# Performance work log

Hardware: AMD Instinct MI355X
Metric: run time of the kernel (lower is better)

Reference implementation:

```python
import jax, jax.numpy as jnp
import numpy as np

N, E, D_IN, D_HID, D_OUT = 50000, 600000, 128, 128, 64


def setup_inputs() -> dict:
    key = jax.random.key(0)
    ks = jax.random.split(key, 8)
    x = jax.random.normal(ks[0], (N, D_IN), dtype=jnp.float32)
    edge_index = jax.random.randint(ks[1], (2, E), 0, N, dtype=jnp.int64)
    def glorot(k, fan_in, fan_out):
        s = (6.0 / (fan_in + fan_out)) ** 0.5
        return jax.random.uniform(k, (fan_in, fan_out), jnp.float32, -s, s)
    return {
        "x": x,
        "W1": glorot(ks[2], D_IN, D_HID), "b1": jnp.zeros((D_HID,), jnp.float32),
        "W2": glorot(ks[3], D_HID, D_HID), "b2": jnp.zeros((D_HID,), jnp.float32),
        "W3": glorot(ks[4], D_HID, D_OUT), "b3": jnp.zeros((D_OUT,), jnp.float32),
        "edge_index": edge_index,
    }


def reference(x, W1, b1, W2, b2, W3, b3, edge_index):
    n = x.shape[0]
    # GCN with self-loops: A_hat = A + I, norm = D^-1/2 A_hat D^-1/2
    loops = jnp.arange(n, dtype=edge_index.dtype)
    row = jnp.concatenate([edge_index[0], loops])  # source nodes
    col = jnp.concatenate([edge_index[1], loops])  # target nodes
    deg = jax.ops.segment_sum(jnp.ones_like(col, dtype=x.dtype), col, num_segments=n)
    dinv = jnp.where(deg > 0, jax.lax.rsqrt(deg), 0.0)
    norm = dinv[row] * dinv[col]  # [E+N]

    def gcn_conv(h, W, b):
        hw = h @ W                                   # [N, out]
        msg = hw[row] * norm[:, None]                # [E+N, out] gather + scale
        return jax.ops.segment_sum(msg, col, num_segments=n) + b

    h = jax.nn.relu(gcn_conv(x, W1, b1))
    h = jax.nn.relu(gcn_conv(h, W2, b2))
    return gcn_conv(h, W3, b3)
```

## Files before the change

### kernel.cpp

```cpp
#include <hip/hip_runtime.h>
#include <hip/hip_bf16.h>
#include <hip/hip_fp16.h>


__device__ inline float4 h4_to_f4(float2 raw) {
    __half2 lo = *reinterpret_cast<__half2*>(&raw.x);
    __half2 hi = *reinterpret_cast<__half2*>(&raw.y);
    float2 a = __half22float2(lo);
    float2 b = __half22float2(hi);
    return make_float4(a.x, a.y, b.x, b.y);
}

__device__ inline float2 f4_to_h4(float4 v) {
    __half2 lo = __floats2half2_rn(v.x, v.y);
    __half2 hi = __floats2half2_rn(v.z, v.w);
    float2 r;
    r.x = *reinterpret_cast<float*>(&lo);
    r.y = *reinterpret_cast<float*>(&hi);
    return r;
}

__global__ __launch_bounds__(256) void zero_counts_kernel(int4* __restrict__ p, int n4) {
    int i = blockIdx.x * 256 + threadIdx.x;
    if (i < n4) p[i] = make_int4(0, 0, 0, 0);
}

__global__ void count_edges_kernel(const int* __restrict__ col, int* __restrict__ counts, int E) {
    int e = blockIdx.x * blockDim.x + threadIdx.x;
    if (e < E) atomicAdd(&counts[col[e]], 1);
}

__global__ __launch_bounds__(256) void block_sum_kernel(const int* __restrict__ counts,
                                                        int* __restrict__ blocksum, int n) {
    int i = blockIdx.x * 256 + threadIdx.x;
    int v = (i < n) ? counts[i] : 0;
    #pragma unroll
    for (int d = 1; d < 64; d <<= 1) v += __shfl_xor(v, d);
    __shared__ int ws[4];
    if ((threadIdx.x & 63) == 0) ws[threadIdx.x >> 6] = v;
    __syncthreads();
    if (threadIdx.x == 0) blocksum[blockIdx.x] = ws[0] + ws[1] + ws[2] + ws[3];
}

__global__ __launch_bounds__(256) void scan_sums_kernel(const int* __restrict__ blocksum,
                                                        int* __restrict__ blockoff,
                                                        int* __restrict__ offsets, int nb, int n) {
    int tid = threadIdx.x;
    int lane = tid & 63, wid = tid >> 6;
    int orig = (tid < nb) ? blocksum[tid] : 0;
    int v = orig;
    #pragma unroll
    for (int d = 1; d < 64; d <<= 1) {
        int u = __shfl_up(v, d);
        if (lane >= d) v += u;
    }
    __shared__ int ws[4];
    if (lane == 63) ws[wid] = v;
    __syncthreads();
    int add = 0;
    for (int w = 0; w < wid; ++w) add += ws[w];
    v += add;
    if (tid < nb) blockoff[tid] = v - orig;
    if (tid == 255) offsets[n] = v;
}

__global__ __launch_bounds__(256) void write_offsets_kernel(const int* __restrict__ counts,
                                                            const int* __restrict__ blockoff,
                                                            int* __restrict__ offsets,
                                                            int* __restrict__ cursor,
                                                            float* __restrict__ dinv, int n) {
    int tid = threadIdx.x;
    int i = blockIdx.x * 256 + tid;
    int lane = tid & 63, wid = tid >> 6;
    int c = (i < n) ? counts[i] : 0;
    int v = c;
    #pragma unroll
    for (int d = 1; d < 64; d <<= 1) {
        int u = __shfl_up(v, d);
        if (lane >= d) v += u;
    }
    __shared__ int ws[4];
    if (lane == 63) ws[wid] = v;
    __syncthreads();
    int add = 0;
    for (int w = 0; w < wid; ++w) add += ws[w];
    int incl = v + add;
    if (i < n) {
        offsets[i] = blockoff[blockIdx.x] + incl - c;
        cursor[i] = 0;
        dinv[i] = rsqrtf((float)(c + 1));
    }
}

__global__ void fill_csr_kernel(const int* __restrict__ row, const int* __restrict__ col,
                                const int* __restrict__ offsets, int* __restrict__ cursor,
                                const float* __restrict__ dinv,
                                int2* __restrict__ edges, int E) {
    int e = blockIdx.x * blockDim.x + threadIdx.x;
    if (e < E) {
        int c = col[e];
        int r = row[e];
        int pos = offsets[c] + atomicAdd(&cursor[c], 1);
        edges[pos] = make_int2(r, __float_as_int(dinv[r] * dinv[c]));
    }
}

template <int DO>
__global__ __launch_bounds__(256, 2) void gemm_kernel(const float* __restrict__ A,
                                                      const float* __restrict__ W,
                                                      __half* __restrict__ out, int n) {
    constexpr int K = 128;
    constexpr int COLTH = DO / 8;
    constexpr int ROWTH = 256 / COLTH;
    constexpr int R = 8;
    constexpr int BR = ROWTH * R;
    constexpr int HALF = DO / 2;

    __shared__ float Wl[K * DO];

    int tid = threadIdx.x;
    #pragma unroll
    for (int q = tid; q < K * DO / 4; q += 256) {
        ((float4*)Wl)[q] = ((const float4*)W)[q];
    }
    __syncthreads();

    int ct = tid % COLTH;
    int rt = tid / COLTH;
    int rb = blockIdx.x * BR + rt * R;

    const float4* A4 = (const float4*)A;

    int rowc[R];
    #pragma unroll
    for (int i = 0; i < R; ++i) {
        int row = rb + i;
        rowc[i] = (row < n) ? row : (n - 1);
    }

    float4 acc[R][2];
    #pragma unroll
    for (int i = 0; i < R; ++i) {
        acc[i][0].x = acc[i][0].y = acc[i][0].z = acc[i][0].w = 0.f;
        acc[i][1].x = acc[i][1].y = acc[i][1].z = acc[i][1].w = 0.f;
    }

    #pragma unroll 2
    for (int k4 = 0; k4 < K / 4; ++k4) {
        float4 areg[R];
        #pragma unroll
        for (int i = 0; i < R; ++i) {
            areg[i] = A4[(size_t)rowc[i] * (K / 4) + k4];
        }
        #pragma unroll
        for (int q = 0; q < 4; ++q) {
            int k = k4 * 4 + q;
            float4 w0 = *(const float4*)(Wl + k * DO + ct * 4);
            float4 w1 = *(const float4*)(Wl + k * DO + HALF + ct * 4);
            #pragma unroll
            for (int i = 0; i < R; ++i) {
                float a = (q == 0) ? areg[i].x : (q == 1) ? areg[i].y
                        : (q == 2) ? areg[i].z : areg[i].w;
                acc[i][0].x += a * w0.x; acc[i][0].y += a * w0.y;
                acc[i][0].z += a * w0.z; acc[i][0].w += a * w0.w;
                acc[i][1].x += a * w1.x; acc[i][1].y += a * w1.y;
                acc[i][1].z += a * w1.z; acc[i][1].w += a * w1.w;
            }
        }
    }

    #pragma unroll
    for (int i = 0; i < R; ++i) {
        int row = rb + i;
        if (row < n) {
            *(float2*)(out + (size_t)row * DO + ct * 4) = f4_to_h4(acc[i][0]);
            *(float2*)(out + (size_t)row * DO + HALF + ct * 4) = f4_to_h4(acc[i][1]);
        }
    }
}

template <int DO, bool RELU>
__global__ __launch_bounds__(256) void agg_kernel(const __half* __restrict__ hw,
                                                  const int* __restrict__ offsets,
                                                  const int2* __restrict__ edges,
                                                  const float* __restrict__ dinv,
                                                  const float* __restrict__ bias,
                                                  float* __restrict__ out, int n) {
    constexpr int TPD = DO / 4;
    constexpr int DPB = 256 / TPD;
    int d = blockIdx.x * DPB + threadIdx.x / TPD;
    int j = threadIdx.x % TPD;
    if (d >= n) return;

    const float2* hw2 = (const float2*)hw;
    int beg = offsets[d];
    int end = offsets[d + 1];
    float di = dinv[d];
    float sw = di * di;

    float4 b4 = ((const float4*)bias)[j];
    float4 self = h4_to_f4(hw2[(size_t)d * TPD + j]);
    float4 acc;
    acc.x = b4.x + self.x * sw;
    acc.y = b4.y + self.y * sw;
    acc.z = b4.z + self.z * sw;
    acc.w = b4.w + self.w * sw;

    int e = beg;
    #define EDGE_FMA(EE) do {                                            \
        int2 er = edges[EE];                                             \
        float w = __int_as_float(er.y);                                  \
        float4 v = h4_to_f4(hw2[(size_t)er.x * TPD + j]);                \
        acc.x += v.x * w; acc.y += v.y * w;                              \
        acc.z += v.z * w; acc.w += v.w * w;                              \
    } while (0)

    for (; e + 8 <= end; e += 8) {
        int2 r0 = edges[e + 0], r1 = edges[e + 1], r2 = edges[e + 2], r3 = edges[e + 3];
        int2 r4 = edges[e + 4], r5 = edges[e + 5], r6 = edges[e + 6], r7 = edges[e + 7];
        float4 v0 = h4_to_f4(hw2[(size_t)r0.x * TPD + j]);
        float4 v1 = h4_to_f4(hw2[(size_t)r1.x * TPD + j]);
        float4 v2 = h4_to_f4(hw2[(size_t)r2.x * TPD + j]);
        float4 v3 = h4_to_f4(hw2[(size_t)r3.x * TPD + j]);
        float4 v4 = h4_to_f4(hw2[(size_t)r4.x * TPD + j]);
        float4 v5 = h4_to_f4(hw2[(size_t)r5.x * TPD + j]);
        float4 v6 = h4_to_f4(hw2[(size_t)r6.x * TPD + j]);
        float4 v7 = h4_to_f4(hw2[(size_t)r7.x * TPD + j]);
        float w0 = __int_as_float(r0.y), w1 = __int_as_float(r1.y);
        float w2 = __int_as_float(r2.y), w3 = __int_as_float(r3.y);
        float w4 = __int_as_float(r4.y), w5 = __int_as_float(r5.y);
        float w6 = __int_as_float(r6.y), w7 = __int_as_float(r7.y);
        acc.x += v0.x * w0; acc.y += v0.y * w0; acc.z += v0.z * w0; acc.w += v0.w * w0;
        acc.x += v1.x * w1; acc.y += v1.y * w1; acc.z += v1.z * w1; acc.w += v1.w * w1;
        acc.x += v2.x * w2; acc.y += v2.y * w2; acc.z += v2.z * w2; acc.w += v2.w * w2;
        acc.x += v3.x * w3; acc.y += v3.y * w3; acc.z += v3.z * w3; acc.w += v3.w * w3;
        acc.x += v4.x * w4; acc.y += v4.y * w4; acc.z += v4.z * w4; acc.w += v4.w * w4;
        acc.x += v5.x * w5; acc.y += v5.y * w5; acc.z += v5.z * w5; acc.w += v5.w * w5;
        acc.x += v6.x * w6; acc.y += v6.y * w6; acc.z += v6.z * w6; acc.w += v6.w * w6;
        acc.x += v7.x * w7; acc.y += v7.y * w7; acc.z += v7.z * w7; acc.w += v7.w * w7;
    }
    for (; e + 4 <= end; e += 4) {
        int2 r0 = edges[e + 0], r1 = edges[e + 1], r2 = edges[e + 2], r3 = edges[e + 3];
        float4 v0 = h4_to_f4(hw2[(size_t)r0.x * TPD + j]);
        float4 v1 = h4_to_f4(hw2[(size_t)r1.x * TPD + j]);
        float4 v2 = h4_to_f4(hw2[(size_t)r2.x * TPD + j]);
        float4 v3 = h4_to_f4(hw2[(size_t)r3.x * TPD + j]);
        float w0 = __int_as_float(r0.y), w1 = __int_as_float(r1.y);
        float w2 = __int_as_float(r2.y), w3 = __int_as_float(r3.y);
        acc.x += v0.x * w0; acc.y += v0.y * w0; acc.z += v0.z * w0; acc.w += v0.w * w0;
        acc.x += v1.x * w1; acc.y += v1.y * w1; acc.z += v1.z * w1; acc.w += v1.w * w1;
        acc.x += v2.x * w2; acc.y += v2.y * w2; acc.z += v2.z * w2; acc.w += v2.w * w2;
        acc.x += v3.x * w3; acc.y += v3.y * w3; acc.z += v3.z * w3; acc.w += v3.w * w3;
    }
    for (; e < end; ++e) EDGE_FMA(e);
    #undef EDGE_FMA

    if (RELU) {
        acc.x = fmaxf(acc.x, 0.f); acc.y = fmaxf(acc.y, 0.f);
        acc.z = fmaxf(acc.z, 0.f); acc.w = fmaxf(acc.w, 0.f);
    }
    ((float4*)out)[(size_t)d * TPD + j] = acc;
}

extern "C" void kernel_launch(void* const* d_in, const int* in_sizes, int n_in,
                              void* d_out, int out_size, void* d_ws, size_t ws_size,
                              hipStream_t stream) {
    const float* x  = (const float*)d_in[0];
    const float* W1 = (const float*)d_in[1];
    const float* b1 = (const float*)d_in[2];
    const float* W2 = (const float*)d_in[3];
    const float* b2 = (const float*)d_in[4];
    const float* W3 = (const float*)d_in[5];
    const float* b3 = (const float*)d_in[6];
    const int*   ei = (const int*)d_in[7];

    const int N = in_sizes[0] / 128;
    const int E = in_sizes[7] / 2;
    const int* rowi = ei;
    const int* coli = ei + E;

    float* out = (float*)d_out;

    char* ws = (char*)d_ws;
    size_t off = 0;
    auto alloc = [&](size_t bytes) -> void* {
        void* p = ws + off;
        off = (off + bytes + 255) & ~(size_t)255;
        return p;
    };
    const int NB = (N + 255) / 256;
    float* dinv     = (float*)alloc((size_t)N * 4);
    int*   counts   = (int*)  alloc(((size_t)N + 4) * 4);
    int*   offsets  = (int*)  alloc((size_t)(N + 1) * 4);
    int*   cursor   = (int*)  alloc((size_t)N * 4);
    int*   blocksum = (int*)  alloc((size_t)NB * 4);
    int*   blockoff = (int*)  alloc((size_t)NB * 4);
    int2*  edges    = (int2*) alloc((size_t)E * 8);
    __half* hw16    = (__half*)alloc((size_t)N * 128 * 2);
    float* hbuf     = (float*)alloc((size_t)N * 128 * 4);

    const int n4 = (N + 3) / 4;
    zero_counts_kernel<<<(n4 + 255) / 256, 256, 0, stream>>>((int4*)counts, n4);
    count_edges_kernel<<<(E + 255) / 256, 256, 0, stream>>>(coli, counts, E);
    block_sum_kernel<<<NB, 256, 0, stream>>>(counts, blocksum, N);
    scan_sums_kernel<<<1, 256, 0, stream>>>(blocksum, blockoff, offsets, NB, N);
    write_offsets_kernel<<<NB, 256, 0, stream>>>(counts, blockoff, offsets, cursor, dinv, N);
    fill_csr_kernel<<<(E + 255) / 256, 256, 0, stream>>>(rowi, coli, offsets, cursor, dinv, edges, E);

    gemm_kernel<128><<<(N + 127) / 128, 256, 0, stream>>>(x, W1, hw16, N);
    agg_kernel<128, true><<<(N + 7) / 8, 256, 0, stream>>>(hw16, offsets, edges, dinv, b1, hbuf, N);

    gemm_kernel<128><<<(N + 127) / 128, 256, 0, stream>>>(hbuf, W2, hw16, N);
    agg_kernel<128, true><<<(N + 7) / 8, 256, 0, stream>>>(hw16, offsets, edges, dinv, b2, hbuf, N);

    gemm_kernel<64><<<(N + 255) / 256, 256, 0, stream>>>(hbuf, W3, hw16, N);
    agg_kernel<64, false><<<(N + 15) / 16, 256, 0, stream>>>(hw16, offsets, edges, dinv, b3, out, N);
}
```

Measured before the change: 234.9 us.

## Run GEMMs in fp16 with fdot2 and store hidden activations as fp16

Converts the input features to fp16 in a separate pass. The GEMMs now read fp16 activations and fp16-packed weights and accumulate in fp32 via packed dot2 instructions. The hidden-layer aggregation kernels write fp16 instead of fp32, which halves activation traffic between layers and roughly halves the GEMM's ALU and LDS cost. In exchange it adds one extra conversion kernel over x and loses precision in the inputs and intermediate activations.

```diff
diff --git a/kernel.cpp b/kernel.cpp
--- a/kernel.cpp
+++ b/kernel.cpp
@@ -2,6 +2,9 @@
 #include <hip/hip_bf16.h>
 #include <hip/hip_fp16.h>
 
+
+typedef _Float16 h2 __attribute__((ext_vector_type(2)));
+typedef _Float16 h8 __attribute__((ext_vector_type(8)));
 
 __device__ inline float4 h4_to_f4(float2 raw) {
     __half2 lo = *reinterpret_cast<__half2*>(&raw.x);
@@ -11,18 +14,23 @@
     return make_float4(a.x, a.y, b.x, b.y);
 }
 
-__device__ inline float2 f4_to_h4(float4 v) {
-    __half2 lo = __floats2half2_rn(v.x, v.y);
-    __half2 hi = __floats2half2_rn(v.z, v.w);
-    float2 r;
-    r.x = *reinterpret_cast<float*>(&lo);
-    r.y = *reinterpret_cast<float*>(&hi);
-    return r;
+__device__ inline uint pack_h2(float a, float b) {
+    __half2 h = __floats2half2_rn(a, b);
+    return *reinterpret_cast<uint*>(&h);
 }
 
 __global__ __launch_bounds__(256) void zero_counts_kernel(int4* __restrict__ p, int n4) {
     int i = blockIdx.x * 256 + threadIdx.x;
     if (i < n4) p[i] = make_int4(0, 0, 0, 0);
+}
+
+__global__ __launch_bounds__(256) void f32_to_f16_kernel(const float4* __restrict__ in,
+                                                         uint2* __restrict__ out, int n4) {
+    int i = blockIdx.x * 256 + threadIdx.x;
+    if (i < n4) {
+        float4 v = in[i];
+        out[i] = make_uint2(pack_h2(v.x, v.y), pack_h2(v.z, v.w));
+    }
 }
 
 __global__ void count_edges_kernel(const int* __restrict__ col, int* __restrict__ counts, int E) {
@@ -106,22 +114,29 @@
 }
 
 template <int DO>
-__global__ __launch_bounds__(256, 2) void gemm_kernel(const float* __restrict__ A,
-                                                      const float* __restrict__ W,
-                                                      __half* __restrict__ out, int n) {
+__global__ __launch_bounds__(256, 2) void gemm16_kernel(const __half* __restrict__ A,
+                                                        const float* __restrict__ W,
+                                                        __half* __restrict__ out, int n) {
     constexpr int K = 128;
     constexpr int COLTH = DO / 8;
     constexpr int ROWTH = 256 / COLTH;
-    constexpr int R = 8;
+    constexpr int R = (DO == 128) ? 8 : 4;
     constexpr int BR = ROWTH * R;
     constexpr int HALF = DO / 2;
 
-    __shared__ float Wl[K * DO];
+    __shared__ alignas(16) h2 Wl[(K / 2) * DO];
 
     int tid = threadIdx.x;
-    #pragma unroll
-    for (int q = tid; q < K * DO / 4; q += 256) {
-        ((float4*)Wl)[q] = ((const float4*)W)[q];
+    for (int idx = tid; idx < (K / 2) * (DO / 4); idx += 256) {
+        int k2 = idx / (DO / 4);
+        int c4 = idx % (DO / 4);
+        float4 w0 = ((const float4*)(W + (size_t)(2 * k2) * DO))[c4];
+        float4 w1 = ((const float4*)(W + (size_t)(2 * k2 + 1) * DO))[c4];
+        h2* dst = &Wl[k2 * DO + c4 * 4];
+        h2 d0; d0.x = (_Float16)w0.x; d0.y = (_Float16)w1.x; dst[0] = d0;
+        h2 d1; d1.x = (_Float16)w0.y; d1.y = (_Float16)w1.y; dst[1] = d1;
+        h2 d2; d2.x = (_Float16)w0.z; d2.y = (_Float16)w1.z; dst[2] = d2;
+        h2 d3; d3.x = (_Float16)w0.w; d3.y = (_Float16)w1.w; dst[3] = d3;
     }
     __syncthreads();
 
@@ -129,8 +144,6 @@
     int rt = tid / COLTH;
     int rb = blockIdx.x * BR + rt * R;
 
-    const float4* A4 = (const float4*)A;
-
     int rowc[R];
     #pragma unroll
     for (int i = 0; i < R; ++i) {
@@ -138,33 +151,33 @@
         rowc[i] = (row < n) ? row : (n - 1);
     }
 
-    float4 acc[R][2];
-    #pragma unroll
-    for (int i = 0; i < R; ++i) {
-        acc[i][0].x = acc[i][0].y = acc[i][0].z = acc[i][0].w = 0.f;
-        acc[i][1].x = acc[i][1].y = acc[i][1].z = acc[i][1].w = 0.f;
-    }
+    float acc[R][8];
+    #pragma unroll
+    for (int i = 0; i < R; ++i)
+        #pragma unroll
+        for (int c = 0; c < 8; ++c) acc[i][c] = 0.f;
 
     #pragma unroll 2
-    for (int k4 = 0; k4 < K / 4; ++k4) {
-        float4 areg[R];
+    for (int k8 = 0; k8 < K / 8; ++k8) {
+        h8 av[R];
         #pragma unroll
         for (int i = 0; i < R; ++i) {
-            areg[i] = A4[(size_t)rowc[i] * (K / 4) + k4];
+            av[i] = ((const h8*)(A + (size_t)rowc[i] * K))[k8];
         }
         #pragma unroll
-        for (int q = 0; q < 4; ++q) {
-            int k = k4 * 4 + q;
-            float4 w0 = *(const float4*)(Wl + k * DO + ct * 4);
-            float4 w1 = *(const float4*)(Wl + k * DO + HALF + ct * 4);
+        for (int kk = 0; kk < 4; ++kk) {
+            int k2 = k8 * 4 + kk;
+            h2 w0[4], w1[4];
+            *(uint4*)w0 = *(const uint4*)(&Wl[k2 * DO + ct * 4]);
+            *(uint4*)w1 = *(const uint4*)(&Wl[k2 * DO + HALF + ct * 4]);
             #pragma unroll
             for (int i = 0; i < R; ++i) {
-                float a = (q == 0) ? areg[i].x : (q == 1) ? areg[i].y
-                        : (q == 2) ? areg[i].z : areg[i].w;
-                acc[i][0].x += a * w0.x; acc[i][0].y += a * w0.y;
-                acc[i][0].z += a * w0.z; acc[i][0].w += a * w0.w;
-                acc[i][1].x += a * w1.x; acc[i][1].y += a * w1.y;
-                acc[i][1].z += a * w1.z; acc[i][1].w += a * w1.w;
+                h2 a; a.x = av[i][2 * kk]; a.y = av[i][2 * kk + 1];
+                #pragma unroll
+                for (int c = 0; c < 4; ++c) {
+                    acc[i][c]     = __builtin_amdgcn_fdot2(a, w0[c], acc[i][c], false);
+                    acc[i][4 + c] = __builtin_amdgcn_fdot2(a, w1[c], acc[i][4 + c], false);
+                }
             }
         }
     }
@@ -173,19 +186,21 @@
     for (int i = 0; i < R; ++i) {
         int row = rb + i;
         if (row < n) {
-            *(float2*)(out + (size_t)row * DO + ct * 4) = f4_to_h4(acc[i][0]);
-            *(float2*)(out + (size_t)row * DO + HALF + ct * 4) = f4_to_h4(acc[i][1]);
+            uint2 q0 = make_uint2(pack_h2(acc[i][0], acc[i][1]), pack_h2(acc[i][2], acc[i][3]));
+            uint2 q1 = make_uint2(pack_h2(acc[i][4], acc[i][5]), pack_h2(acc[i][6], acc[i][7]));
+            *(uint2*)(out + (size_t)row * DO + ct * 4) = q0;
+            *(uint2*)(out + (size_t)row * DO + HALF + ct * 4) = q1;
         }
     }
 }
 
-template <int DO, bool RELU>
+template <int DO, bool RELU, bool F16OUT>
 __global__ __launch_bounds__(256) void agg_kernel(const __half* __restrict__ hw,
                                                   const int* __restrict__ offsets,
                                                   const int2* __restrict__ edges,
                                                   const float* __restrict__ dinv,
                                                   const float* __restrict__ bias,
-                                                  float* __restrict__ out, int n) {
+                                                  void* __restrict__ outp, int n) {
     constexpr int TPD = DO / 4;
     constexpr int DPB = 256 / TPD;
     int d = blockIdx.x * DPB + threadIdx.x / TPD;
@@ -207,14 +222,6 @@
     acc.w = b4.w + self.w * sw;
 
     int e = beg;
-    #define EDGE_FMA(EE) do {                                            \
-        int2 er = edges[EE];                                             \
-        float w = __int_as_float(er.y);                                  \
-        float4 v = h4_to_f4(hw2[(size_t)er.x * TPD + j]);                \
-        acc.x += v.x * w; acc.y += v.y * w;                              \
-        acc.z += v.z * w; acc.w += v.w * w;                              \
-    } while (0)
-
     for (; e + 8 <= end; e += 8) {
         int2 r0 = edges[e + 0], r1 = edges[e + 1], r2 = edges[e + 2], r3 = edges[e + 3];
         int2 r4 = edges[e + 4], r5 = edges[e + 5], r6 = edges[e + 6], r7 = edges[e + 7];
@@ -252,14 +259,23 @@
         acc.x += v2.x * w2; acc.y += v2.y * w2; acc.z += v2.z * w2; acc.w += v2.w * w2;
         acc.x += v3.x * w3; acc.y += v3.y * w3; acc.z += v3.z * w3; acc.w += v3.w * w3;
     }
-    for (; e < end; ++e) EDGE_FMA(e);
-    #undef EDGE_FMA
+    for (; e < end; ++e) {
+        int2 er = edges[e];
+        float w = __int_as_float(er.y);
+        float4 v = h4_to_f4(hw2[(size_t)er.x * TPD + j]);
+        acc.x += v.x * w; acc.y += v.y * w; acc.z += v.z * w; acc.w += v.w * w;
+    }
 
     if (RELU) {
         acc.x = fmaxf(acc.x, 0.f); acc.y = fmaxf(acc.y, 0.f);
         acc.z = fmaxf(acc.z, 0.f); acc.w = fmaxf(acc.w, 0.f);
     }
-    ((float4*)out)[(size_t)d * TPD + j] = acc;
+    if (F16OUT) {
+        uint2 q = make_uint2(pack_h2(acc.x, acc.y), pack_h2(acc.z, acc.w));
+        ((uint2*)outp)[(size_t)d * TPD + j] = q;
+    } else {
+        ((float4*)outp)[(size_t)d * TPD + j] = acc;
+    }
 }
 
 extern "C" void kernel_launch(void* const* d_in, const int* in_sizes, int n_in,
@@ -296,8 +312,9 @@
     int*   blocksum = (int*)  alloc((size_t)NB * 4);
     int*   blockoff = (int*)  alloc((size_t)NB * 4);
     int2*  edges    = (int2*) alloc((size_t)E * 8);
+    __half* x16     = (__half*)alloc((size_t)N * 128 * 2);
     __half* hw16    = (__half*)alloc((size_t)N * 128 * 2);
-    float* hbuf     = (float*)alloc((size_t)N * 128 * 4);
+    __half* h16     = (__half*)alloc((size_t)N * 128 * 2);
 
     const int n4 = (N + 3) / 4;
     zero_counts_kernel<<<(n4 + 255) / 256, 256, 0, stream>>>((int4*)counts, n4);
@@ -306,13 +323,15 @@
     scan_sums_kernel<<<1, 256, 0, stream>>>(blocksum, blockoff, offsets, NB, N);
     write_offsets_kernel<<<NB, 256, 0, stream>>>(counts, blockoff, offsets, cursor, dinv, N);
     fill_csr_kernel<<<(E + 255) / 256, 256, 0, stream>>>(rowi, coli, offsets, cursor, dinv, edges, E);
-
-    gemm_kernel<128><<<(N + 127) / 128, 256, 0, stream>>>(x, W1, hw16, N);
-    agg_kernel<128, true><<<(N + 7) / 8, 256, 0, stream>>>(hw16, offsets, edges, dinv, b1, hbuf, N);
-
-    gemm_kernel<128><<<(N + 127) / 128, 256, 0, stream>>>(hbuf, W2, hw16, N);
-    agg_kernel<128, true><<<(N + 7) / 8, 256, 0, stream>>>(hw16, offsets, edges, dinv, b2, hbuf, N);
-
-    gemm_kernel<64><<<(N + 255) / 256, 256, 0, stream>>>(hbuf, W3, hw16, N);
-    agg_kernel<64, false><<<(N + 15) / 16, 256, 0, stream>>>(hw16, offsets, edges, dinv, b3, out, N);
-}
+    const int xc4 = N * 128 / 4;
+    f32_to_f16_kernel<<<(xc4 + 255) / 256, 256, 0, stream>>>((const float4*)x, (uint2*)x16, xc4);
+
+    gemm16_kernel<128><<<(N + 127) / 128, 256, 0, stream>>>(x16, W1, hw16, N);
+    agg_kernel<128, true, true><<<(N + 7) / 8, 256, 0, stream>>>(hw16, offsets, edges, dinv, b1, h16, N);
+
+    gemm16_kernel<128><<<(N + 127) / 128, 256, 0, stream>>>(h16, W2, hw16, N);
+    agg_kernel<128, true, true><<<(N + 7) / 8, 256, 0, stream>>>(hw16, offsets, edges, dinv, b2, h16, N);
+
+    gemm16_kernel<64><<<(N + 127) / 128, 256, 0, stream>>>(h16, W3, hw16, N);
+    agg_kernel<64, false, false><<<(N + 15) / 16, 256, 0, stream>>>(hw16, offsets, edges, dinv, b3, out, N);
+}
```

After: 221.0 us. 5.9% less time.
